# Kernel tuning notes

Measured on AMD Instinct MI355X. Metric: run time of the kernel, lower is better.

## Reference

```python
import jax, jax.numpy as jnp
import numpy as np

GRID = 25
NUM_NODE = GRID * GRID  # 625, hard-coded by the original module

def _neighbor_flat_indices():
    # Replicates the torch index construction exactly, incl. boundary shifts.
    offsets = np.array([[-1,-1],[-1,0],[-1,1],[0,-1],[0,0],[0,1],[1,-1],[1,0],[1,1]])
    idx = np.arange(NUM_NODE)
    rows = idx // GRID
    cols = idx % GRID
    nr = rows[:, None] + offsets[:, 0]   # [625, 9]
    nc = cols[:, None] + offsets[:, 1]
    nr = nr.reshape(GRID, GRID, 9)
    nr[0, :, :] += 1                     # reflect top boundary
    nr[-1, :, :] -= 1                    # reflect bottom boundary
    nr = nr.reshape(NUM_NODE, 9)
    nc = nc.reshape(GRID, GRID, 9)
    nc[:, 0, :] += 1                     # reflect left boundary
    nc[:, -1, :] -= 1                    # reflect right boundary
    nc = nc.reshape(NUM_NODE, 9)
    return jnp.asarray(nr * GRID + nc)   # [625, 9] flat node indices

NEIGH = _neighbor_flat_indices()

def setup_inputs() -> dict:
    key = jax.random.key(0)
    k1, k2, k3, k4, k5 = jax.random.split(key, 5)
    B = 512
    x = jax.random.normal(k1, (B, NUM_NODE, 66), dtype=jnp.float32)
    # nn.Linear(66, 64): weight [64, 66], bias [64]
    W_fc = jax.random.normal(k2, (64, 66), dtype=jnp.float32) * (1.0 / np.sqrt(66))
    b_fc = jax.random.normal(k3, (64,), dtype=jnp.float32) * 0.01
    # nn.Linear(128, 1): weight [1, 128], bias [1]
    W_at = jax.random.normal(k4, (1, 128), dtype=jnp.float32) * (1.0 / np.sqrt(128))
    b_at = jax.random.normal(k5, (1,), dtype=jnp.float32) * 0.01
    return {"x": x, "W_fc": W_fc, "b_fc": b_fc, "W_at": W_at, "b_at": b_at}

def reference(x, W_fc, b_fc, W_at, b_at):
    # h = fc(x): [B, 625, 64]
    h = jnp.einsum('bnf,df->bnd', x, W_fc) + b_fc
    # Gather fixed 9-neighbor features: [B, 625, 9, 64]
    x2 = h[:, NEIGH, :]
    # Center feature broadcast to the 9 neighbor slots: [B, 625, 9, 64]
    x1 = jnp.broadcast_to(h[:, :, None, :], x2.shape)
    z = jnp.concatenate([x1, x2], axis=-1)                  # [B, 625, 9, 128]
    s = jnp.einsum('bnkf,of->bnko', z, W_at) + b_at          # [B, 625, 9, 1]
    s = jax.nn.leaky_relu(s, negative_slope=0.01)[..., 0]    # [B, 625, 9]
    # exp(s) / sum(exp(s)) over the 9 neighbors == softmax(s)
    attn_weight = jax.nn.softmax(s, axis=-1)                 # [B, 625, 9]
    # Original: sum_k h[:, :, None, :] * w[..., None] over k
    # = h * sum_k w  (h does not depend on k); avoids a [B,625,9,64] temp.
    attn_vector = h * jnp.sum(attn_weight, axis=-1, keepdims=True)  # [B, 625, 64]
    return (attn_vector, attn_weight)
```

## Files before the change

kernel.cpp:

```cpp
#include <hip/hip_runtime.h>

#define BATCH 512
#define GRID_N 25
#define NODES 625
#define BN (BATCH * NODES)
#define NTILES (BN / 16)
#define F 66
#define D 64
#define WPB 4
#define NT_GRP WPB
#define GROUP_F (NT_GRP * 16 * F)
#define WAVE_F (16 * F)
#define G_PER_BLK 5
#define NBLOCKS_P (NTILES / (NT_GRP * G_PER_BLK))

#define LOADS_PG  5
#define STORES_PG 18

typedef short bf16x8 __attribute__((ext_vector_type(8)));
typedef float f32x4  __attribute__((ext_vector_type(4)));

__device__ __forceinline__ short f2bf(float f) {
    union { float f; unsigned u; } c; c.f = f;
    unsigned r = c.u + 0x7fffu + ((c.u >> 16) & 1u);
    return (short)(r >> 16);
}

typedef const __attribute__((address_space(1))) void gas_void;
typedef __attribute__((address_space(3))) void las_void;
__device__ __forceinline__ void gload_lds16(const float* g, float* l) {
    __builtin_amdgcn_global_load_lds((gas_void*)g, (las_void*)l, 16, 0, 0);
}

__global__ __launch_bounds__(256, 4) void fc_mfma(
    const float* __restrict__ x, const float* __restrict__ Wfc,
    const float* __restrict__ bfc, const float* __restrict__ Wat,
    float* __restrict__ hout, float* __restrict__ u, float* __restrict__ v)
{
    const int tid  = threadIdx.x;
    const int lane = tid & 63;
    const int wid  = tid >> 6;
    const int l15  = lane & 15;
    const int quad = lane >> 4;

    __shared__ float stage[2][WPB][WAVE_F];

    const int gbase = blockIdx.x * G_PER_BLK;

    {
        const float* src = x + (size_t)gbase * GROUP_F + wid * WAVE_F;
        float* dst = &stage[0][wid][0];
#pragma unroll
        for (int r = 0; r < 4; ++r)
            gload_lds16(src + r * 256 + lane * 4, dst + r * 256);
        if (lane < 8)
            gload_lds16(src + 1024 + lane * 4, dst + 1024);
    }

    bf16x8 bfrag[4][3];
#pragma unroll
    for (int t = 0; t < 4; ++t) {
        const float2* wr = (const float2*)Wfc + (t * 16 + l15) * 33;
#pragma unroll
        for (int c = 0; c < 2; ++c) {
            bf16x8 fr;
#pragma unroll
            for (int j2 = 0; j2 < 4; ++j2) {
                const float2 p = wr[c * 16 + quad * 4 + j2];
                fr[j2 * 2]     = f2bf(p.x);
                fr[j2 * 2 + 1] = f2bf(p.y);
            }
            bfrag[t][c] = fr;
        }
        bf16x8 z = {0, 0, 0, 0, 0, 0, 0, 0};
        if (quad == 0) {
            const float2 p = wr[32];
            z[0] = f2bf(p.x); z[1] = f2bf(p.y);
        }
        bfrag[t][2] = z;
    }
    float bft[4], wa1[4], wa2[4];
#pragma unroll
    for (int t = 0; t < 4; ++t) {
        bft[t] = bfc[t * 16 + l15];
        wa1[t] = Wat[t * 16 + l15];
        wa2[t] = Wat[64 + t * 16 + l15];
    }

    for (int g = 0; g < G_PER_BLK; ++g) {
        const int s = g & 1;

        if (g + 1 < G_PER_BLK) {
            const float* src = x + (size_t)(gbase + g + 1) * GROUP_F + wid * WAVE_F;
            float* dst = &stage[s ^ 1][wid][0];
#pragma unroll
            for (int r = 0; r < 4; ++r)
                gload_lds16(src + r * 256 + lane * 4, dst + r * 256);
            if (lane < 8)
                gload_lds16(src + 1024 + lane * 4, dst + 1024);
        }
        if (g == 0)
            asm volatile("s_waitcnt vmcnt(5)" ::: "memory");
        else if (g + 1 < G_PER_BLK)
            asm volatile("s_waitcnt vmcnt(23)" ::: "memory");
        else
            asm volatile("s_waitcnt vmcnt(18)" ::: "memory");
        __builtin_amdgcn_sched_barrier(0);

        const float2* wbase = (const float2*)&stage[s][wid][0];
        const int bn0 = ((gbase + g) * NT_GRP + wid) * 16;

        const float2* rp = wbase + l15 * 33 + quad * 4;
        bf16x8 afrag[3];
#pragma unroll
        for (int c = 0; c < 2; ++c) {
            bf16x8 fr;
#pragma unroll
            for (int j2 = 0; j2 < 4; ++j2) {
                const float2 p = rp[c * 16 + j2];
                fr[j2 * 2]     = f2bf(p.x);
                fr[j2 * 2 + 1] = f2bf(p.y);
            }
            afrag[c] = fr;
        }
        {
            bf16x8 z = {0, 0, 0, 0, 0, 0, 0, 0};
            if (quad == 0) {
                const float2 p = wbase[l15 * 33 + 32];
                z[0] = f2bf(p.x); z[1] = f2bf(p.y);
            }
            afrag[2] = z;
        }

        f32x4 acc[4] = {{0,0,0,0},{0,0,0,0},{0,0,0,0},{0,0,0,0}};
#pragma unroll
        for (int nt = 0; nt < 4; ++nt)
#pragma unroll
            for (int c = 0; c < 3; ++c)
                acc[nt] = __builtin_amdgcn_mfma_f32_16x16x32_bf16(afrag[c], bfrag[nt][c], acc[nt], 0, 0, 0);

        float pu[4] = {0, 0, 0, 0}, pv[4] = {0, 0, 0, 0};
#pragma unroll
        for (int nt = 0; nt < 4; ++nt) {
#pragma unroll
            for (int r = 0; r < 4; ++r) {
                const float h = acc[nt][r] + bft[nt];
                hout[(size_t)(bn0 + quad * 4 + r) * D + nt * 16 + l15] = h;
                pu[r] = fmaf(h, wa1[nt], pu[r]);
                pv[r] = fmaf(h, wa2[nt], pv[r]);
            }
        }
#pragma unroll
        for (int off = 8; off > 0; off >>= 1) {
#pragma unroll
            for (int r = 0; r < 4; ++r) {
                pu[r] += __shfl_xor(pu[r], off, 64);
                pv[r] += __shfl_xor(pv[r], off, 64);
            }
        }
        if (l15 == 0) {
            *(float4*)(u + bn0 + quad * 4) = make_float4(pu[0], pu[1], pu[2], pu[3]);
            *(float4*)(v + bn0 + quad * 4) = make_float4(pv[0], pv[1], pv[2], pv[3]);
        }
    }
}

__global__ __launch_bounds__(256) void attn_kernel(
    const float* __restrict__ u, const float* __restrict__ v,
    const float* __restrict__ bat, float* __restrict__ wout)
{
    __shared__ float sw[256 * 9];
    const int tid  = threadIdx.x;
    const int lane = tid & 63;
    const int wid  = tid >> 6;
    const int bn   = blockIdx.x * 256 + tid;

    const int b   = bn / NODES;
    const int n   = bn - b * NODES;
    const int row = n / GRID_N;
    const int col = n - row * GRID_N;
    const int r0 = row + (row == 0) - (row == GRID_N - 1);
    const int c0 = col + (col == 0) - (col == GRID_N - 1);

    const float* vb = v + b * NODES;
    const float u0 = u[bn] + bat[0];

    float s[9];
#pragma unroll
    for (int k = 0; k < 9; ++k) {
        const int nr = r0 + (k / 3) - 1;
        const int nc = c0 + (k % 3) - 1;
        const float t = u0 + vb[nr * GRID_N + nc];
        s[k] = (t >= 0.0f) ? t : 0.01f * t;
    }
    float m = s[0];
#pragma unroll
    for (int k = 1; k < 9; ++k) m = fmaxf(m, s[k]);
    float sum = 0.0f;
#pragma unroll
    for (int k = 0; k < 9; ++k) { s[k] = __expf(s[k] - m); sum += s[k]; }
    const float inv = 1.0f / sum;

    float* ws = sw + wid * 576;
#pragma unroll
    for (int k = 0; k < 9; ++k) ws[lane * 9 + k] = s[k] * inv;

    float4* dst = (float4*)(wout + (size_t)(blockIdx.x * 256 + wid * 64) * 9);
    const float4* src = (const float4*)ws;
    dst[lane]      = src[lane];
    dst[64 + lane] = src[64 + lane];
    if (lane < 16) dst[128 + lane] = src[128 + lane];
}

extern "C" void kernel_launch(void* const* d_in, const int* in_sizes, int n_in,
                              void* d_out, int out_size, void* d_ws, size_t ws_size,
                              hipStream_t stream)
{
    const float* x   = (const float*)d_in[0];
    const float* Wfc = (const float*)d_in[1];
    const float* bfc = (const float*)d_in[2];
    const float* Wat = (const float*)d_in[3];
    const float* bat = (const float*)d_in[4];

    float* hout = (float*)d_out;
    float* wout = (float*)d_out + (size_t)BN * D;
    float* u = (float*)d_ws;
    float* v = u + BN;

    fc_mfma<<<NBLOCKS_P, 256, 0, stream>>>(x, Wfc, bfc, Wat, hout, u, v);
    attn_kernel<<<BN / 256, 256, 0, stream>>>(u, v, bat, wout);
}
```

Measured before the change: 182.2 us.

## Fuse FC and attention softmax into one per-batch kernel using LDS u/v

Merges the two kernels into one launch where each 512-thread block handles one batch element. The block computes h and the u/v projections for all 625 nodes, keeps u/v in LDS, then runs the 9-neighbour softmax from LDS and writes the weights out. This removes the global u/v round trip and the second launch. The last tile overlaps the previous one (starting at node 609) to cover the 625-node remainder. The cost is a grid of only 512 blocks with 8 waves each, a different load pipeline depth, and a block-wide sync before the softmax phase.

```diff
diff --git a/kernel.cpp b/kernel.cpp
--- a/kernel.cpp
+++ b/kernel.cpp
@@ -4,18 +4,14 @@
 #define GRID_N 25
 #define NODES 625
 #define BN (BATCH * NODES)
-#define NTILES (BN / 16)
 #define F 66
 #define D 64
-#define WPB 4
-#define NT_GRP WPB
-#define GROUP_F (NT_GRP * 16 * F)
+#define WPB 8
+#define TPW 5
+#define NT 40
 #define WAVE_F (16 * F)
-#define G_PER_BLK 5
-#define NBLOCKS_P (NTILES / (NT_GRP * G_PER_BLK))
-
-#define LOADS_PG  5
-#define STORES_PG 18
+#define TAIL_TS (NODES - 16)
+
 
 typedef short bf16x8 __attribute__((ext_vector_type(8)));
 typedef float f32x4  __attribute__((ext_vector_type(4)));
@@ -32,23 +28,27 @@
     __builtin_amdgcn_global_load_lds((gas_void*)g, (las_void*)l, 16, 0, 0);
 }
 
-__global__ __launch_bounds__(256, 4) void fc_mfma(
+__global__ __launch_bounds__(512, 2) void fused(
     const float* __restrict__ x, const float* __restrict__ Wfc,
     const float* __restrict__ bfc, const float* __restrict__ Wat,
-    float* __restrict__ hout, float* __restrict__ u, float* __restrict__ v)
+    const float* __restrict__ bat,
+    float* __restrict__ hout, float* __restrict__ wout)
 {
     const int tid  = threadIdx.x;
     const int lane = tid & 63;
     const int wid  = tid >> 6;
     const int l15  = lane & 15;
     const int quad = lane >> 4;
+    const int b    = blockIdx.x;
 
     __shared__ float stage[2][WPB][WAVE_F];
-
-    const int gbase = blockIdx.x * G_PER_BLK;
+    __shared__ float u_lds[640];
+    __shared__ float v_lds[640];
+
+    const float* xb = x + (size_t)b * NODES * F;
 
     {
-        const float* src = x + (size_t)gbase * GROUP_F + wid * WAVE_F;
+        const float* src = xb + (size_t)(wid * TPW * 16) * F;
         float* dst = &stage[0][wid][0];
 #pragma unroll
         for (int r = 0; r < 4; ++r)
@@ -57,6 +57,8 @@
             gload_lds16(src + 1024 + lane * 4, dst + 1024);
     }
 
+    const float bat0 = bat[0];
+
     bf16x8 bfrag[4][3];
 #pragma unroll
     for (int t = 0; t < 4; ++t) {
@@ -87,11 +89,13 @@
         wa2[t] = Wat[64 + t * 16 + l15];
     }
 
-    for (int g = 0; g < G_PER_BLK; ++g) {
-        const int s = g & 1;
-
-        if (g + 1 < G_PER_BLK) {
-            const float* src = x + (size_t)(gbase + g + 1) * GROUP_F + wid * WAVE_F;
+    for (int t = 0; t < TPW; ++t) {
+        const int s = t & 1;
+
+        if (t + 1 < TPW) {
+            const int tile = wid * TPW + t + 1;
+            const int ts   = (tile == NT - 1) ? TAIL_TS : tile * 16;
+            const float* src = xb + (size_t)ts * F;
             float* dst = &stage[s ^ 1][wid][0];
 #pragma unroll
             for (int r = 0; r < 4; ++r)
@@ -99,16 +103,17 @@
             if (lane < 8)
                 gload_lds16(src + 1024 + lane * 4, dst + 1024);
         }
-        if (g == 0)
+        if (t == 0)
             asm volatile("s_waitcnt vmcnt(5)" ::: "memory");
-        else if (g + 1 < G_PER_BLK)
-            asm volatile("s_waitcnt vmcnt(23)" ::: "memory");
+        else if (t + 1 < TPW)
+            asm volatile("s_waitcnt vmcnt(21)" ::: "memory");
         else
-            asm volatile("s_waitcnt vmcnt(18)" ::: "memory");
+            asm volatile("s_waitcnt vmcnt(16)" ::: "memory");
         __builtin_amdgcn_sched_barrier(0);
 
+        const int tile = wid * TPW + t;
+        const int ts   = (tile == NT - 1) ? TAIL_TS : tile * 16;
         const float2* wbase = (const float2*)&stage[s][wid][0];
-        const int bn0 = ((gbase + g) * NT_GRP + wid) * 16;
 
         const float2* rp = wbase + l15 * 33 + quad * 4;
         bf16x8 afrag[3];
@@ -139,13 +144,14 @@
             for (int c = 0; c < 3; ++c)
                 acc[nt] = __builtin_amdgcn_mfma_f32_16x16x32_bf16(afrag[c], bfrag[nt][c], acc[nt], 0, 0, 0);
 
+        const size_t gn0 = (size_t)b * NODES + ts;
         float pu[4] = {0, 0, 0, 0}, pv[4] = {0, 0, 0, 0};
 #pragma unroll
         for (int nt = 0; nt < 4; ++nt) {
 #pragma unroll
             for (int r = 0; r < 4; ++r) {
                 const float h = acc[nt][r] + bft[nt];
-                hout[(size_t)(bn0 + quad * 4 + r) * D + nt * 16 + l15] = h;
+                hout[(gn0 + quad * 4 + r) * D + nt * 16 + l15] = h;
                 pu[r] = fmaf(h, wa1[nt], pu[r]);
                 pv[r] = fmaf(h, wa2[nt], pv[r]);
             }
@@ -159,57 +165,51 @@
             }
         }
         if (l15 == 0) {
-            *(float4*)(u + bn0 + quad * 4) = make_float4(pu[0], pu[1], pu[2], pu[3]);
-            *(float4*)(v + bn0 + quad * 4) = make_float4(pv[0], pv[1], pv[2], pv[3]);
-        }
-    }
-}
-
-__global__ __launch_bounds__(256) void attn_kernel(
-    const float* __restrict__ u, const float* __restrict__ v,
-    const float* __restrict__ bat, float* __restrict__ wout)
-{
-    __shared__ float sw[256 * 9];
-    const int tid  = threadIdx.x;
-    const int lane = tid & 63;
-    const int wid  = tid >> 6;
-    const int bn   = blockIdx.x * 256 + tid;
-
-    const int b   = bn / NODES;
-    const int n   = bn - b * NODES;
-    const int row = n / GRID_N;
-    const int col = n - row * GRID_N;
-    const int r0 = row + (row == 0) - (row == GRID_N - 1);
-    const int c0 = col + (col == 0) - (col == GRID_N - 1);
-
-    const float* vb = v + b * NODES;
-    const float u0 = u[bn] + bat[0];
-
-    float s[9];
-#pragma unroll
-    for (int k = 0; k < 9; ++k) {
-        const int nr = r0 + (k / 3) - 1;
-        const int nc = c0 + (k % 3) - 1;
-        const float t = u0 + vb[nr * GRID_N + nc];
-        s[k] = (t >= 0.0f) ? t : 0.01f * t;
-    }
-    float m = s[0];
-#pragma unroll
-    for (int k = 1; k < 9; ++k) m = fmaxf(m, s[k]);
-    float sum = 0.0f;
-#pragma unroll
-    for (int k = 0; k < 9; ++k) { s[k] = __expf(s[k] - m); sum += s[k]; }
-    const float inv = 1.0f / sum;
-
-    float* ws = sw + wid * 576;
-#pragma unroll
-    for (int k = 0; k < 9; ++k) ws[lane * 9 + k] = s[k] * inv;
-
-    float4* dst = (float4*)(wout + (size_t)(blockIdx.x * 256 + wid * 64) * 9);
-    const float4* src = (const float4*)ws;
-    dst[lane]      = src[lane];
-    dst[64 + lane] = src[64 + lane];
-    if (lane < 16) dst[128 + lane] = src[128 + lane];
+#pragma unroll
+            for (int r = 0; r < 4; ++r) {
+                u_lds[ts + quad * 4 + r] = pu[r];
+                v_lds[ts + quad * 4 + r] = pv[r];
+            }
+        }
+    }
+
+    __syncthreads();
+
+    float* sw = &stage[0][0][0];
+#pragma unroll
+    for (int rnd = 0; rnd < 2; ++rnd) {
+        const int ln = tid + rnd * 512;
+        if (ln < NODES) {
+            const int row = ln / GRID_N;
+            const int col = ln - row * GRID_N;
+            const int r0 = row + (row == 0) - (row == GRID_N - 1);
+            const int c0 = col + (col == 0) - (col == GRID_N - 1);
+            const float u0 = u_lds[ln] + bat0;
+
+            float sv[9];
+#pragma unroll
+            for (int k = 0; k < 9; ++k) {
+                const int nr = r0 + (k / 3) - 1;
+                const int nc = c0 + (k % 3) - 1;
+                const float tt = u0 + v_lds[nr * GRID_N + nc];
+                sv[k] = (tt >= 0.0f) ? tt : 0.01f * tt;
+            }
+            float m = sv[0];
+#pragma unroll
+            for (int k = 1; k < 9; ++k) m = fmaxf(m, sv[k]);
+            float sum = 0.0f;
+#pragma unroll
+            for (int k = 0; k < 9; ++k) { sv[k] = __expf(sv[k] - m); sum += sv[k]; }
+            const float inv = 1.0f / sum;
+#pragma unroll
+            for (int k = 0; k < 9; ++k) sw[ln * 9 + k] = sv[k] * inv;
+        }
+    }
+    __syncthreads();
+
+    float* wb = wout + (size_t)b * (NODES * 9);
+    for (int i = tid; i < NODES * 9; i += 512)
+        wb[i] = sw[i];
 }
 
 extern "C" void kernel_launch(void* const* d_in, const int* in_sizes, int n_in,
@@ -224,9 +224,6 @@
 
     float* hout = (float*)d_out;
     float* wout = (float*)d_out + (size_t)BN * D;
-    float* u = (float*)d_ws;
-    float* v = u + BN;
-
-    fc_mfma<<<NBLOCKS_P, 256, 0, stream>>>(x, Wfc, bfc, Wat, hout, u, v);
-    attn_kernel<<<BN / 256, 256, 0, stream>>>(u, v, bat, wout);
-}
+
+    fused<<<BATCH, 512, 0, stream>>>(x, Wfc, bfc, Wat, bat, hout, wout);
+}
```

Measured after the change: 172.7 us. -5.2%, faster.
